# Performance work log

Measured on AMD Instinct MI355X. Metric: run time of the kernel, lower is better.

Reference implementation:

```python
import jax, jax.numpy as jnp
import numpy as np

K, D, H, PD = 512, 512, 512, 128  # nodes, input_dim(=hidden), hidden_dim, pair_dim
P = K * (K - 1)
EPS = 1e-5


def setup_inputs() -> dict:
    key = jax.random.key(0)
    ks = jax.random.split(key, 16)
    s = lambda n: 1.0 / np.sqrt(n)
    return {
        "x": jax.random.normal(ks[0], (K, D), jnp.float32),
        "pair_feats": jax.random.normal(ks[1], (P, PD), jnp.float32),
        "W_att": jax.random.normal(ks[2], (1, 2 * D + PD), jnp.float32) * s(2 * D + PD),
        "b_att": jnp.zeros((1,), jnp.float32),
        "W_obj": jax.random.normal(ks[3], (H, D), jnp.float32) * s(D),
        "b_obj": jnp.zeros((H,), jnp.float32),
        "W_pair": jax.random.normal(ks[4], (H, PD), jnp.float32) * s(PD),
        "b_pair": jnp.zeros((H,), jnp.float32),
        "ln_g": jnp.ones((H,), jnp.float32),
        "ln_b": jnp.zeros((H,), jnp.float32),
        "W1": jax.random.normal(ks[5], (H, H), jnp.float32) * s(H),
        "b1": jnp.zeros((H,), jnp.float32),
        "W2": jax.random.normal(ks[6], (H, H), jnp.float32) * s(H),
        "b2": jnp.zeros((H,), jnp.float32),
    }


def _layernorm(v, g, b):
    mu = jnp.mean(v, axis=-1, keepdims=True)
    var = jnp.mean(jnp.square(v - mu), axis=-1, keepdims=True)
    return g * (v - mu) * jax.lax.rsqrt(var + EPS) + b


def reference(x, pair_feats, W_att, b_att, W_obj, b_obj, W_pair, b_pair,
              ln_g, ln_b, W1, b1, W2, b2):
    k = x.shape[0]
    # j index for each (i, slot t): j = t + (t >= i), i.e. all j != i, ascending
    t = jnp.arange(k - 1)
    j_idx = t[None, :] + (t[None, :] >= jnp.arange(k)[:, None])  # [K, K-1]

    # split the att_mlp weight to avoid materializing cat([x_i, x_j, pair])
    wa, wb, wc = W_att[0, :D], W_att[0, D:2 * D], W_att[0, 2 * D:]
    sa = x @ wa                                           # [K]
    sb = x @ wb                                           # [K]
    pf = pair_feats.reshape(k, k - 1, PD)                 # row-major (i, j!=i)
    sc = jnp.einsum('ktp,p->kt', pf, wc)                  # [K, K-1]
    alpha = jax.nn.sigmoid(sa[:, None] + sb[j_idx] + sc + b_att[0])  # [K, K-1]

    oj = x @ W_obj.T + b_obj                              # [K, H]
    pp = jnp.einsum('ktp,hp->kth', pf, W_pair) + b_pair   # [K, K-1, H]
    messages = jnp.mean(alpha[..., None] * (oj[j_idx] + pp), axis=1)  # [K, H]

    out = _layernorm(x + messages, ln_g, ln_b)
    ffn = jax.nn.relu(out @ W1.T + b1) @ W2.T + b2
    out = _layernorm(out + ffn, ln_g, ln_b)
    return out
```

## Files before the change

### kernel.cpp

```cpp
#include <hip/hip_runtime.h>
#include <math.h>

#define KK 512
#define DD 512
#define HH 512
#define PD 128
#define KM1 511
#define LN_EPS 1e-5f
#define NCHUNK 4
#define CHUNK_T 128

typedef __attribute__((ext_vector_type(8))) short sh8;
typedef __attribute__((ext_vector_type(4))) short sh4;
typedef __attribute__((ext_vector_type(4))) float fx4;

#define MFMA16(a, b, c) __builtin_amdgcn_mfma_f32_16x16x32_bf16(a, b, c, 0, 0, 0)

__device__ __forceinline__ float wave_reduce_sum(float v) {
    #pragma unroll
    for (int off = 32; off > 0; off >>= 1)
        v += __shfl_xor(v, off, 64);
    return v;
}

__device__ __forceinline__ float half_reduce_sum(float v) {
    #pragma unroll
    for (int off = 16; off > 0; off >>= 1)
        v += __shfl_xor(v, off, 64);
    return v;
}

__device__ __forceinline__ short f2bf(float f) {
    unsigned u = __float_as_uint(f);
    u += 0x7fff + ((u >> 16) & 1);
    return (short)(u >> 16);
}

__device__ __forceinline__ sh8 load_cvt8(const float* p) {
    float4 v0 = *(const float4*)p;
    float4 v1 = *(const float4*)(p + 4);
    sh8 r;
    r[0] = f2bf(v0.x); r[1] = f2bf(v0.y); r[2] = f2bf(v0.z); r[3] = f2bf(v0.w);
    r[4] = f2bf(v1.x); r[5] = f2bf(v1.y); r[6] = f2bf(v1.z); r[7] = f2bf(v1.w);
    return r;
}

__global__ __launch_bounds__(256) void prep_sab(
    const float* __restrict__ W_obj, const float* __restrict__ W_pair,
    const float* __restrict__ W1, const float* __restrict__ W2,
    short* __restrict__ W_objb, short* __restrict__ W_pairb,
    short* __restrict__ W1b, short* __restrict__ W2b,
    const float* __restrict__ x, short* __restrict__ xTb,
    const float* __restrict__ W_att, float* __restrict__ sa, float* __restrict__ sb) {
    int bid = blockIdx.x;
    int tid = threadIdx.x;
    if (bid < 832) {
        int i = bid * 256 + tid;
        const float* src; short* dst; int j;
        if (i < 65536)       { src = W_obj;  dst = W_objb;  j = i; }
        else if (i < 81920)  { src = W_pair; dst = W_pairb; j = i - 65536; }
        else if (i < 147456) { src = W1;     dst = W1b;     j = i - 81920; }
        else                 { src = W2;     dst = W2b;     j = i - 147456; }
        float4 v = ((const float4*)src)[j];
        sh4 s;
        s[0] = f2bf(v.x); s[1] = f2bf(v.y); s[2] = f2bf(v.z); s[3] = f2bf(v.w);
        ((sh4*)dst)[j] = s;
    } else if (bid < 1088) {
        int tb = bid - 832;
        int r0 = (tb >> 4) * 32, c0 = (tb & 15) * 32;
        int tx = tid & 31, ty = tid >> 5;
        __shared__ short tileT[32][33];
        #pragma unroll
        for (int i = 0; i < 4; i++) {
            int r = ty + i * 8;
            tileT[tx][r] = f2bf(x[(size_t)(r0 + r) * DD + c0 + tx]);
        }
        __syncthreads();
        #pragma unroll
        for (int i = 0; i < 4; i++) {
            int rr = ty + i * 8;
            xTb[(size_t)(c0 + rr) * KK + r0 + tx] = tileT[rr][tx];
        }
    } else {
        int w = tid >> 6, lane = tid & 63;
        int k = (bid - 1088) * 4 + w;
        const float4* xr = (const float4*)(x + (size_t)k * DD);
        const float4* wa = (const float4*)(W_att);
        const float4* wb = (const float4*)(W_att + DD);
        float pa = 0.f, pb = 0.f;
        #pragma unroll
        for (int i = 0; i < 2; i++) {
            float4 xv = xr[lane + i * 64];
            float4 av = wa[lane + i * 64];
            float4 bv = wb[lane + i * 64];
            pa += xv.x * av.x + xv.y * av.y + xv.z * av.z + xv.w * av.w;
            pb += xv.x * bv.x + xv.y * bv.y + xv.z * bv.z + xv.w * bv.w;
        }
        pa = wave_reduce_sum(pa);
        pb = wave_reduce_sum(pb);
        if (lane == 0) { sa[k] = pa; sb[k] = pb; }
    }
}

__global__ __launch_bounds__(512) void pair_pass_kernel(
    const float* __restrict__ pf, const float* __restrict__ sa,
    const float* __restrict__ sb, const float* __restrict__ W_att,
    const float* __restrict__ b_att, short* __restrict__ Ab,
    float* __restrict__ apf_part, float* __restrict__ asum_part) {
    int k = blockIdx.x;
    int chunk = blockIdx.y;
    int tbase = chunk * CHUNK_T;
    int tid = threadIdx.x;
    int w = tid >> 6, lane = tid & 63;
    int h = lane >> 5, c = lane & 31;
    int g = w * 2 + h;

    float4 wc4 = ((const float4*)(W_att + 2 * DD))[c];
    float sak = sa[k];
    float batt = b_att[0];
    const float4* pfk = (const float4*)(pf + (size_t)k * KM1 * PD);

    float4 v[8];
    int tr[8];
    #pragma unroll
    for (int it = 0; it < 8; it++) {
        int t = tbase + it * 16 + g;
        tr[it] = t;
        int tc = t < KM1 ? t : KM1 - 1;
        v[it] = pfk[(size_t)tc * 32 + c];
    }

    __shared__ float alpha_s[CHUNK_T];
    float a0 = 0.f, a1 = 0.f, a2 = 0.f, a3 = 0.f, asl = 0.f;
    #pragma unroll
    for (int it = 0; it < 8; it++) {
        float part = v[it].x * wc4.x + v[it].y * wc4.y + v[it].z * wc4.z + v[it].w * wc4.w;
        part = half_reduce_sum(part);
        int t = tr[it];
        int j = t + (t >= k);
        int jj = j < KK ? j : KK - 1;
        float z = sak + sb[jj] + part + batt;
        float alpha = (t < KM1) ? 1.f / (1.f + __expf(-z)) : 0.f;
        if (c == 0) alpha_s[it * 16 + g] = alpha;
        a0 += alpha * v[it].x;
        a1 += alpha * v[it].y;
        a2 += alpha * v[it].z;
        a3 += alpha * v[it].w;
        asl += alpha;
    }

    __shared__ float apf_s[16][128];
    __shared__ float asum_s[16];
    apf_s[g][4 * c + 0] = a0;
    apf_s[g][4 * c + 1] = a1;
    apf_s[g][4 * c + 2] = a2;
    apf_s[g][4 * c + 3] = a3;
    if (c == 0) asum_s[g] = asl;
    __syncthreads();
    if (tid < PD) {
        float s = 0.f;
        #pragma unroll
        for (int i = 0; i < 16; i++) s += apf_s[i][tid];
        apf_part[((size_t)chunk * KK + k) * PD + tid] = s;
    }
    if (tid < CHUNK_T) {
        int tt = tbase + tid;
        if (tt < KM1) {
            int j = tt + (tt >= k);
            Ab[(size_t)k * KK + j] = f2bf(alpha_s[tid]);
        }
    }
    if (tid == 0) {
        float s = 0.f;
        #pragma unroll
        for (int i = 0; i < 16; i++) s += asum_s[i];
        asum_part[(size_t)chunk * KK + k] = s;
        if (chunk == 0) Ab[(size_t)k * KK + k] = 0;
    }
}

__global__ __launch_bounds__(128) void k_y(const short* __restrict__ Ab,
                                           const short* __restrict__ xTb,
                                           short* __restrict__ yb) {
    int m0 = blockIdx.y * 32, n0 = blockIdx.x * 32;
    int tid = threadIdx.x;
    int wv = tid >> 6, l = tid & 63;
    int lr = l & 15, lk = (l >> 4) * 8;
    int mw = m0 + wv * 16;
    fx4 acc[2] = {};
    for (int k0 = 0; k0 < KK; k0 += 32) {
        sh8 a  = *(const sh8*)&Ab[(size_t)(mw + lr) * KK + k0 + lk];
        sh8 b0 = *(const sh8*)&xTb[(size_t)(n0 + lr) * KK + k0 + lk];
        sh8 b1 = *(const sh8*)&xTb[(size_t)(n0 + 16 + lr) * KK + k0 + lk];
        acc[0] = MFMA16(a, b0, acc[0]);
        acc[1] = MFMA16(a, b1, acc[1]);
    }
    __shared__ short tile[32][40];
    int lm4 = (l >> 4) * 4;
    #pragma unroll
    for (int cf = 0; cf < 2; cf++)
        #pragma unroll
        for (int r = 0; r < 4; r++)
            tile[wv * 16 + lm4 + r][cf * 16 + lr] = f2bf(acc[cf][r]);
    __syncthreads();
    int row = tid >> 2, co = (tid & 3) * 8;
    *(sh8*)&yb[(size_t)(m0 + row) * KK + n0 + co] = *(sh8*)&tile[row][co];
}

__global__ __launch_bounds__(128) void k_msg(const short* __restrict__ yb,
                                             const short* __restrict__ W_objb,
                                             const float* __restrict__ apf_part,
                                             const short* __restrict__ W_pairb,
                                             float* __restrict__ msg) {
    int m0 = blockIdx.y * 32, n0 = blockIdx.x * 32;
    int tid = threadIdx.x;
    int wv = tid >> 6, l = tid & 63;
    int lr = l & 15, lk = (l >> 4) * 8;
    int mw = m0 + wv * 16;
    fx4 acc[2] = {};
    for (int k0 = 0; k0 < KK; k0 += 32) {
        sh8 a  = *(const sh8*)&yb[(size_t)(mw + lr) * KK + k0 + lk];
        sh8 b0 = *(const sh8*)&W_objb[(size_t)(n0 + lr) * DD + k0 + lk];
        sh8 b1 = *(const sh8*)&W_objb[(size_t)(n0 + 16 + lr) * DD + k0 + lk];
        acc[0] = MFMA16(a, b0, acc[0]);
        acc[1] = MFMA16(a, b1, acc[1]);
    }
    for (int k0 = 0; k0 < PD; k0 += 32) {
        int p = k0 + lk;
        int row = mw + lr;
        float4 u0 = make_float4(0.f, 0.f, 0.f, 0.f);
        float4 u1 = make_float4(0.f, 0.f, 0.f, 0.f);
        #pragma unroll
        for (int cc = 0; cc < NCHUNK; cc++) {
            const float* pp = &apf_part[((size_t)cc * KK + row) * PD + p];
            float4 w0 = *(const float4*)pp;
            float4 w1 = *(const float4*)(pp + 4);
            u0.x += w0.x; u0.y += w0.y; u0.z += w0.z; u0.w += w0.w;
            u1.x += w1.x; u1.y += w1.y; u1.z += w1.z; u1.w += w1.w;
        }
        sh8 a;
        a[0] = f2bf(u0.x); a[1] = f2bf(u0.y); a[2] = f2bf(u0.z); a[3] = f2bf(u0.w);
        a[4] = f2bf(u1.x); a[5] = f2bf(u1.y); a[6] = f2bf(u1.z); a[7] = f2bf(u1.w);
        sh8 b0 = *(const sh8*)&W_pairb[(size_t)(n0 + lr) * PD + p];
        sh8 b1 = *(const sh8*)&W_pairb[(size_t)(n0 + 16 + lr) * PD + p];
        acc[0] = MFMA16(a, b0, acc[0]);
        acc[1] = MFMA16(a, b1, acc[1]);
    }
    __shared__ float tile[32][36];
    int lm4 = (l >> 4) * 4;
    #pragma unroll
    for (int cf = 0; cf < 2; cf++)
        #pragma unroll
        for (int r = 0; r < 4; r++)
            tile[wv * 16 + lm4 + r][cf * 16 + lr] = acc[cf][r];
    __syncthreads();
    for (int q = tid; q < 256; q += 128) {
        int row = q >> 3, c4 = q & 7;
        *(float4*)&msg[(size_t)(m0 + row) * HH + n0 + c4 * 4] = *(float4*)&tile[row][c4 * 4];
    }
}

__global__ __launch_bounds__(128) void ln1_kernel(
    const float* __restrict__ msg, const float* __restrict__ x,
    const float* __restrict__ asum_part, const float* __restrict__ b_pair,
    const float* __restrict__ b_obj, const float* __restrict__ ln_g,
    const float* __restrict__ ln_b, float* __restrict__ out1,
    short* __restrict__ out1b) {
    int k = blockIdx.x;
    int tid = threadIdx.x;
    int wv = tid >> 6, l = tid & 63;
    float as = asum_part[k] + asum_part[KK + k] + asum_part[2 * KK + k] + asum_part[3 * KK + k];
    float4 m  = ((const float4*)(msg + (size_t)k * HH))[tid];
    float4 bp = ((const float4*)b_pair)[tid];
    float4 bo = ((const float4*)b_obj)[tid];
    float4 xr = ((const float4*)(x + (size_t)k * DD))[tid];
    const float inv = 1.0f / (float)KM1;
    float4 v;
    v.x = xr.x + (m.x + as * (bp.x + bo.x)) * inv;
    v.y = xr.y + (m.y + as * (bp.y + bo.y)) * inv;
    v.z = xr.z + (m.z + as * (bp.z + bo.z)) * inv;
    v.w = xr.w + (m.w + as * (bp.w + bo.w)) * inv;
    float s1 = v.x + v.y + v.z + v.w;
    float s2 = v.x * v.x + v.y * v.y + v.z * v.z + v.w * v.w;
    s1 = wave_reduce_sum(s1);
    s2 = wave_reduce_sum(s2);
    __shared__ float r1[2], r2[2];
    if (l == 0) { r1[wv] = s1; r2[wv] = s2; }
    __syncthreads();
    float S1 = r1[0] + r1[1], S2 = r2[0] + r2[1];
    float mu = S1 * (1.0f / HH);
    float var = S2 * (1.0f / HH) - mu * mu;
    float rs = rsqrtf(var + LN_EPS);
    float4 g4 = ((const float4*)ln_g)[tid];
    float4 b4 = ((const float4*)ln_b)[tid];
    float4 o;
    o.x = g4.x * (v.x - mu) * rs + b4.x;
    o.y = g4.y * (v.y - mu) * rs + b4.y;
    o.z = g4.z * (v.z - mu) * rs + b4.z;
    o.w = g4.w * (v.w - mu) * rs + b4.w;
    ((float4*)(out1 + (size_t)k * HH))[tid] = o;
    sh4 s;
    s[0] = f2bf(o.x); s[1] = f2bf(o.y); s[2] = f2bf(o.z); s[3] = f2bf(o.w);
    ((sh4*)(out1b + (size_t)k * HH))[tid] = s;
}

__global__ __launch_bounds__(128) void k_ffn1(const short* __restrict__ out1b,
                                              const short* __restrict__ W1b,
                                              const float* __restrict__ b1,
                                              short* __restrict__ h1b) {
    int m0 = blockIdx.y * 32, n0 = blockIdx.x * 32;
    int tid = threadIdx.x;
    int wv = tid >> 6, l = tid & 63;
    int lr = l & 15, lk = (l >> 4) * 8;
    int mw = m0 + wv * 16;
    fx4 acc[2] = {};
    for (int k0 = 0; k0 < HH; k0 += 32) {
        sh8 a  = *(const sh8*)&out1b[(size_t)(mw + lr) * HH + k0 + lk];
        sh8 b0 = *(const sh8*)&W1b[(size_t)(n0 + lr) * HH + k0 + lk];
        sh8 b1 = *(const sh8*)&W1b[(size_t)(n0 + 16 + lr) * HH + k0 + lk];
        acc[0] = MFMA16(a, b0, acc[0]);
        acc[1] = MFMA16(a, b1, acc[1]);
    }
    __shared__ short tile[32][40];
    int lm4 = (l >> 4) * 4;
    #pragma unroll
    for (int cf = 0; cf < 2; cf++) {
        int col = cf * 16 + lr;
        float bb = b1[n0 + col];
        #pragma unroll
        for (int r = 0; r < 4; r++)
            tile[wv * 16 + lm4 + r][col] = f2bf(fmaxf(acc[cf][r] + bb, 0.f));
    }
    __syncthreads();
    int row = tid >> 2, co = (tid & 3) * 8;
    *(sh8*)&h1b[(size_t)(m0 + row) * HH + n0 + co] = *(sh8*)&tile[row][co];
}

__global__ __launch_bounds__(128) void k_ffn2(const short* __restrict__ h1b,
                                              const short* __restrict__ W2b,
                                              float* __restrict__ ffn) {
    int m0 = blockIdx.y * 32, n0 = blockIdx.x * 32;
    int tid = threadIdx.x;
    int wv = tid >> 6, l = tid & 63;
    int lr = l & 15, lk = (l >> 4) * 8;
    int mw = m0 + wv * 16;
    fx4 acc[2] = {};
    for (int k0 = 0; k0 < HH; k0 += 32) {
        sh8 a  = *(const sh8*)&h1b[(size_t)(mw + lr) * HH + k0 + lk];
        sh8 b0 = *(const sh8*)&W2b[(size_t)(n0 + lr) * HH + k0 + lk];
        sh8 b1 = *(const sh8*)&W2b[(size_t)(n0 + 16 + lr) * HH + k0 + lk];
        acc[0] = MFMA16(a, b0, acc[0]);
        acc[1] = MFMA16(a, b1, acc[1]);
    }
    __shared__ float tile[32][36];
    int lm4 = (l >> 4) * 4;
    #pragma unroll
    for (int cf = 0; cf < 2; cf++)
        #pragma unroll
        for (int r = 0; r < 4; r++)
            tile[wv * 16 + lm4 + r][cf * 16 + lr] = acc[cf][r];
    __syncthreads();
    for (int q = tid; q < 256; q += 128) {
        int row = q >> 3, c4 = q & 7;
        *(float4*)&ffn[(size_t)(m0 + row) * HH + n0 + c4 * 4] = *(float4*)&tile[row][c4 * 4];
    }
}

__global__ __launch_bounds__(128) void ln2_kernel(
    const float* __restrict__ ffn, const float* __restrict__ out1,
    const float* __restrict__ b2, const float* __restrict__ ln_g,
    const float* __restrict__ ln_b, float* __restrict__ out) {
    int k = blockIdx.x;
    int tid = threadIdx.x;
    int wv = tid >> 6, l = tid & 63;
    float4 f  = ((const float4*)(ffn + (size_t)k * HH))[tid];
    float4 xr = ((const float4*)(out1 + (size_t)k * HH))[tid];
    float4 bb = ((const float4*)b2)[tid];
    float4 v;
    v.x = xr.x + f.x + bb.x;
    v.y = xr.y + f.y + bb.y;
    v.z = xr.z + f.z + bb.z;
    v.w = xr.w + f.w + bb.w;
    float s1 = v.x + v.y + v.z + v.w;
    float s2 = v.x * v.x + v.y * v.y + v.z * v.z + v.w * v.w;
    s1 = wave_reduce_sum(s1);
    s2 = wave_reduce_sum(s2);
    __shared__ float r1[2], r2[2];
    if (l == 0) { r1[wv] = s1; r2[wv] = s2; }
    __syncthreads();
    float S1 = r1[0] + r1[1], S2 = r2[0] + r2[1];
    float mu = S1 * (1.0f / HH);
    float var = S2 * (1.0f / HH) - mu * mu;
    float rs = rsqrtf(var + LN_EPS);
    float4 g4 = ((const float4*)ln_g)[tid];
    float4 b4 = ((const float4*)ln_b)[tid];
    float4 o;
    o.x = g4.x * (v.x - mu) * rs + b4.x;
    o.y = g4.y * (v.y - mu) * rs + b4.y;
    o.z = g4.z * (v.z - mu) * rs + b4.z;
    o.w = g4.w * (v.w - mu) * rs + b4.w;
    ((float4*)(out + (size_t)k * HH))[tid] = o;
}

extern "C" void kernel_launch(void* const* d_in, const int* in_sizes, int n_in,
                              void* d_out, int out_size, void* d_ws, size_t ws_size,
                              hipStream_t stream) {
    const float* x          = (const float*)d_in[0];
    const float* pair_feats = (const float*)d_in[1];
    const float* W_att      = (const float*)d_in[2];
    const float* b_att      = (const float*)d_in[3];
    const float* W_obj      = (const float*)d_in[4];
    const float* b_obj      = (const float*)d_in[5];
    const float* W_pair     = (const float*)d_in[6];
    const float* b_pair     = (const float*)d_in[7];
    const float* ln_g       = (const float*)d_in[8];
    const float* ln_b       = (const float*)d_in[9];
    const float* W1         = (const float*)d_in[10];
    const float* b1         = (const float*)d_in[11];
    const float* W2         = (const float*)d_in[12];
    const float* b2         = (const float*)d_in[13];
    float* out = (float*)d_out;

    const size_t MAT = (size_t)KK * HH;
    float* ws        = (float*)d_ws;
    float* sa        = ws;
    float* sb        = sa + KK;
    float* asum_part = sb + KK;
    float* apf_part  = asum_part + NCHUNK * KK;
    float* msg       = apf_part + (size_t)NCHUNK * KK * PD;
    float* out1      = msg + MAT;
    float* ffn       = out1 + MAT;
    float* psink     = ffn + MAT;
    short* Ab        = (short*)(psink + NCHUNK * KK);
    short* xTb       = Ab + MAT;
    short* W_objb    = xTb + MAT;
    short* W_pairb   = W_objb + MAT;
    short* W1b       = W_pairb + (size_t)HH * PD;
    short* W2b       = W1b + MAT;
    short* yb        = W2b + MAT;
    short* out1b     = yb + MAT;
    short* h1b       = out1b + MAT;

    prep_sab<<<1216, 256, 0, stream>>>(W_obj, W_pair, W1, W2, W_objb, W_pairb, W1b, W2b,
                                       x, xTb, W_att, sa, sb);
    pair_pass_kernel<<<dim3(512, NCHUNK), 512, 0, stream>>>(pair_feats, sa, sb, W_att, b_att,
                                                            Ab, apf_part, asum_part);
    k_y<<<dim3(16, 16), 128, 0, stream>>>(Ab, xTb, yb);
    k_msg<<<dim3(16, 16), 128, 0, stream>>>(yb, W_objb, apf_part, W_pairb, msg);
    ln1_kernel<<<512, 128, 0, stream>>>(msg, x, asum_part, b_pair, b_obj, ln_g, ln_b, out1, out1b);
    k_ffn1<<<dim3(16, 16), 128, 0, stream>>>(out1b, W1b, b1, h1b);
    k_ffn2<<<dim3(16, 16), 128, 0, stream>>>(h1b, W2b, ffn);
    ln2_kernel<<<512, 128, 0, stream>>>(ffn, out1, b2, ln_g, ln_b, out);
}
```

Measured before the change: 63.00 us.

## Fuse LayerNorm1 into FFN1 and convert weights to bf16 inside GEMMs

Drops the separate weight-to-bf16 conversion pass; the GEMM kernels now load fp32 weights and convert them in registers. LayerNorm1 is folded into the FFN1 prologue: each block recomputes the normalized rows into shared memory. The final kernel recomputes LN1 from msg so it can apply the residual and LN2 without storing out1. This removes two launches and several intermediate buffers, at the cost of redundant LN1 work across the 16 column blocks and doubled fp32 weight traffic per GEMM tile.

Result: slower. 87.99 us (+39.7%).

```diff
diff --git a/kernel.cpp b/kernel.cpp
--- a/kernel.cpp
+++ b/kernel.cpp
@@ -46,28 +46,12 @@
 }
 
 __global__ __launch_bounds__(256) void prep_sab(
-    const float* __restrict__ W_obj, const float* __restrict__ W_pair,
-    const float* __restrict__ W1, const float* __restrict__ W2,
-    short* __restrict__ W_objb, short* __restrict__ W_pairb,
-    short* __restrict__ W1b, short* __restrict__ W2b,
     const float* __restrict__ x, short* __restrict__ xTb,
     const float* __restrict__ W_att, float* __restrict__ sa, float* __restrict__ sb) {
     int bid = blockIdx.x;
     int tid = threadIdx.x;
-    if (bid < 832) {
-        int i = bid * 256 + tid;
-        const float* src; short* dst; int j;
-        if (i < 65536)       { src = W_obj;  dst = W_objb;  j = i; }
-        else if (i < 81920)  { src = W_pair; dst = W_pairb; j = i - 65536; }
-        else if (i < 147456) { src = W1;     dst = W1b;     j = i - 81920; }
-        else                 { src = W2;     dst = W2b;     j = i - 147456; }
-        float4 v = ((const float4*)src)[j];
-        sh4 s;
-        s[0] = f2bf(v.x); s[1] = f2bf(v.y); s[2] = f2bf(v.z); s[3] = f2bf(v.w);
-        ((sh4*)dst)[j] = s;
-    } else if (bid < 1088) {
-        int tb = bid - 832;
-        int r0 = (tb >> 4) * 32, c0 = (tb & 15) * 32;
+    if (bid < 256) {
+        int r0 = (bid >> 4) * 32, c0 = (bid & 15) * 32;
         int tx = tid & 31, ty = tid >> 5;
         __shared__ short tileT[32][33];
         #pragma unroll
@@ -83,7 +67,7 @@
         }
     } else {
         int w = tid >> 6, lane = tid & 63;
-        int k = (bid - 1088) * 4 + w;
+        int k = (bid - 256) * 4 + w;
         const float4* xr = (const float4*)(x + (size_t)k * DD);
         const float4* wa = (const float4*)(W_att);
         const float4* wb = (const float4*)(W_att + DD);
@@ -208,9 +192,9 @@
 }
 
 __global__ __launch_bounds__(128) void k_msg(const short* __restrict__ yb,
-                                             const short* __restrict__ W_objb,
+                                             const float* __restrict__ W_obj,
                                              const float* __restrict__ apf_part,
-                                             const short* __restrict__ W_pairb,
+                                             const float* __restrict__ W_pair,
                                              float* __restrict__ msg) {
     int m0 = blockIdx.y * 32, n0 = blockIdx.x * 32;
     int tid = threadIdx.x;
@@ -220,8 +204,8 @@
     fx4 acc[2] = {};
     for (int k0 = 0; k0 < KK; k0 += 32) {
         sh8 a  = *(const sh8*)&yb[(size_t)(mw + lr) * KK + k0 + lk];
-        sh8 b0 = *(const sh8*)&W_objb[(size_t)(n0 + lr) * DD + k0 + lk];
-        sh8 b1 = *(const sh8*)&W_objb[(size_t)(n0 + 16 + lr) * DD + k0 + lk];
+        sh8 b0 = load_cvt8(&W_obj[(size_t)(n0 + lr) * DD + k0 + lk]);
+        sh8 b1 = load_cvt8(&W_obj[(size_t)(n0 + 16 + lr) * DD + k0 + lk]);
         acc[0] = MFMA16(a, b0, acc[0]);
         acc[1] = MFMA16(a, b1, acc[1]);
     }
@@ -241,8 +225,8 @@
         sh8 a;
         a[0] = f2bf(u0.x); a[1] = f2bf(u0.y); a[2] = f2bf(u0.z); a[3] = f2bf(u0.w);
         a[4] = f2bf(u1.x); a[5] = f2bf(u1.y); a[6] = f2bf(u1.z); a[7] = f2bf(u1.w);
-        sh8 b0 = *(const sh8*)&W_pairb[(size_t)(n0 + lr) * PD + p];
-        sh8 b1 = *(const sh8*)&W_pairb[(size_t)(n0 + 16 + lr) * PD + p];
+        sh8 b0 = load_cvt8(&W_pair[(size_t)(n0 + lr) * PD + p]);
+        sh8 b1 = load_cvt8(&W_pair[(size_t)(n0 + 16 + lr) * PD + p]);
         acc[0] = MFMA16(a, b0, acc[0]);
         acc[1] = MFMA16(a, b1, acc[1]);
     }
@@ -260,12 +244,126 @@
     }
 }
 
-__global__ __launch_bounds__(128) void ln1_kernel(
+__global__ __launch_bounds__(128) void k_ffn1(
     const float* __restrict__ msg, const float* __restrict__ x,
     const float* __restrict__ asum_part, const float* __restrict__ b_pair,
     const float* __restrict__ b_obj, const float* __restrict__ ln_g,
-    const float* __restrict__ ln_b, float* __restrict__ out1,
-    short* __restrict__ out1b) {
+    const float* __restrict__ ln_b, const float* __restrict__ W1,
+    const float* __restrict__ b1, short* __restrict__ h1b) {
+    int m0 = blockIdx.y * 32, n0 = blockIdx.x * 32;
+    int tid = threadIdx.x;
+    __shared__ short a_tile[32][514];
+
+    {
+        int r = tid >> 2, q = tid & 3;
+        int grow = m0 + r;
+        float as = asum_part[grow] + asum_part[KK + grow] +
+                   asum_part[2 * KK + grow] + asum_part[3 * KK + grow];
+        const float4* m4  = (const float4*)(msg + (size_t)grow * HH);
+        const float4* x4  = (const float4*)(x + (size_t)grow * DD);
+        const float4* bp4 = (const float4*)b_pair;
+        const float4* bo4 = (const float4*)b_obj;
+        const float inv = 1.0f / (float)KM1;
+        float s1 = 0.f, s2 = 0.f;
+        #pragma unroll 8
+        for (int i = 0; i < 32; i++) {
+            int idx = q + i * 4;
+            float4 m = m4[idx], xr = x4[idx], bp = bp4[idx], bo = bo4[idx];
+            float vx = xr.x + (m.x + as * (bp.x + bo.x)) * inv;
+            float vy = xr.y + (m.y + as * (bp.y + bo.y)) * inv;
+            float vz = xr.z + (m.z + as * (bp.z + bo.z)) * inv;
+            float vw = xr.w + (m.w + as * (bp.w + bo.w)) * inv;
+            s1 += vx + vy + vz + vw;
+            s2 += vx * vx + vy * vy + vz * vz + vw * vw;
+        }
+        s1 += __shfl_xor(s1, 1, 64); s1 += __shfl_xor(s1, 2, 64);
+        s2 += __shfl_xor(s2, 1, 64); s2 += __shfl_xor(s2, 2, 64);
+        float mu = s1 * (1.0f / HH);
+        float var = s2 * (1.0f / HH) - mu * mu;
+        float rs = rsqrtf(var + LN_EPS);
+        const float4* g4p = (const float4*)ln_g;
+        const float4* b4p = (const float4*)ln_b;
+        #pragma unroll 8
+        for (int i = 0; i < 32; i++) {
+            int idx = q + i * 4;
+            float4 m = m4[idx], xr = x4[idx], bp = bp4[idx], bo = bo4[idx];
+            float4 g = g4p[idx], bl = b4p[idx];
+            float vx = xr.x + (m.x + as * (bp.x + bo.x)) * inv;
+            float vy = xr.y + (m.y + as * (bp.y + bo.y)) * inv;
+            float vz = xr.z + (m.z + as * (bp.z + bo.z)) * inv;
+            float vw = xr.w + (m.w + as * (bp.w + bo.w)) * inv;
+            sh4 o;
+            o[0] = f2bf(g.x * (vx - mu) * rs + bl.x);
+            o[1] = f2bf(g.y * (vy - mu) * rs + bl.y);
+            o[2] = f2bf(g.z * (vz - mu) * rs + bl.z);
+            o[3] = f2bf(g.w * (vw - mu) * rs + bl.w);
+            *(sh4*)&a_tile[r][idx * 4] = o;
+        }
+    }
+    __syncthreads();
+
+    int wv = tid >> 6, l = tid & 63;
+    int lr = l & 15, lk = (l >> 4) * 8;
+    fx4 acc[2] = {};
+    for (int k0 = 0; k0 < HH; k0 += 32) {
+        sh8 a  = *(const sh8*)&a_tile[wv * 16 + lr][k0 + lk];
+        sh8 b0 = load_cvt8(&W1[(size_t)(n0 + lr) * HH + k0 + lk]);
+        sh8 b1v = load_cvt8(&W1[(size_t)(n0 + 16 + lr) * HH + k0 + lk]);
+        acc[0] = MFMA16(a, b0, acc[0]);
+        acc[1] = MFMA16(a, b1v, acc[1]);
+    }
+    __syncthreads();
+    __shared__ short tile[32][40];
+    int lm4 = (l >> 4) * 4;
+    #pragma unroll
+    for (int cf = 0; cf < 2; cf++) {
+        int col = cf * 16 + lr;
+        float bb = b1[n0 + col];
+        #pragma unroll
+        for (int r = 0; r < 4; r++)
+            tile[wv * 16 + lm4 + r][col] = f2bf(fmaxf(acc[cf][r] + bb, 0.f));
+    }
+    __syncthreads();
+    int row = tid >> 2, co = (tid & 3) * 8;
+    *(sh8*)&h1b[(size_t)(m0 + row) * HH + n0 + co] = *(sh8*)&tile[row][co];
+}
+
+__global__ __launch_bounds__(128) void k_ffn2(const short* __restrict__ h1b,
+                                              const float* __restrict__ W2,
+                                              float* __restrict__ ffn) {
+    int m0 = blockIdx.y * 32, n0 = blockIdx.x * 32;
+    int tid = threadIdx.x;
+    int wv = tid >> 6, l = tid & 63;
+    int lr = l & 15, lk = (l >> 4) * 8;
+    int mw = m0 + wv * 16;
+    fx4 acc[2] = {};
+    for (int k0 = 0; k0 < HH; k0 += 32) {
+        sh8 a  = *(const sh8*)&h1b[(size_t)(mw + lr) * HH + k0 + lk];
+        sh8 b0 = load_cvt8(&W2[(size_t)(n0 + lr) * HH + k0 + lk]);
+        sh8 b1 = load_cvt8(&W2[(size_t)(n0 + 16 + lr) * HH + k0 + lk]);
+        acc[0] = MFMA16(a, b0, acc[0]);
+        acc[1] = MFMA16(a, b1, acc[1]);
+    }
+    __shared__ float tile[32][36];
+    int lm4 = (l >> 4) * 4;
+    #pragma unroll
+    for (int cf = 0; cf < 2; cf++)
+        #pragma unroll
+        for (int r = 0; r < 4; r++)
+            tile[wv * 16 + lm4 + r][cf * 16 + lr] = acc[cf][r];
+    __syncthreads();
+    for (int q = tid; q < 256; q += 128) {
+        int row = q >> 3, c4 = q & 7;
+        *(float4*)&ffn[(size_t)(m0 + row) * HH + n0 + c4 * 4] = *(float4*)&tile[row][c4 * 4];
+    }
+}
+
+__global__ __launch_bounds__(128) void ln2_rec(
+    const float* __restrict__ msg, const float* __restrict__ x,
+    const float* __restrict__ asum_part, const float* __restrict__ b_pair,
+    const float* __restrict__ b_obj, const float* __restrict__ ffn,
+    const float* __restrict__ b2, const float* __restrict__ ln_g,
+    const float* __restrict__ ln_b, float* __restrict__ out) {
     int k = blockIdx.x;
     int tid = threadIdx.x;
     int wv = tid >> 6, l = tid & 63;
@@ -275,13 +373,13 @@
     float4 bo = ((const float4*)b_obj)[tid];
     float4 xr = ((const float4*)(x + (size_t)k * DD))[tid];
     const float inv = 1.0f / (float)KM1;
-    float4 v;
-    v.x = xr.x + (m.x + as * (bp.x + bo.x)) * inv;
-    v.y = xr.y + (m.y + as * (bp.y + bo.y)) * inv;
-    v.z = xr.z + (m.z + as * (bp.z + bo.z)) * inv;
-    v.w = xr.w + (m.w + as * (bp.w + bo.w)) * inv;
-    float s1 = v.x + v.y + v.z + v.w;
-    float s2 = v.x * v.x + v.y * v.y + v.z * v.z + v.w * v.w;
+    float4 v1;
+    v1.x = xr.x + (m.x + as * (bp.x + bo.x)) * inv;
+    v1.y = xr.y + (m.y + as * (bp.y + bo.y)) * inv;
+    v1.z = xr.z + (m.z + as * (bp.z + bo.z)) * inv;
+    v1.w = xr.w + (m.w + as * (bp.w + bo.w)) * inv;
+    float s1 = v1.x + v1.y + v1.z + v1.w;
+    float s2 = v1.x * v1.x + v1.y * v1.y + v1.z * v1.z + v1.w * v1.w;
     s1 = wave_reduce_sum(s1);
     s2 = wave_reduce_sum(s2);
     __shared__ float r1[2], r2[2];
@@ -293,112 +391,35 @@
     float rs = rsqrtf(var + LN_EPS);
     float4 g4 = ((const float4*)ln_g)[tid];
     float4 b4 = ((const float4*)ln_b)[tid];
+    float4 o1;
+    o1.x = g4.x * (v1.x - mu) * rs + b4.x;
+    o1.y = g4.y * (v1.y - mu) * rs + b4.y;
+    o1.z = g4.z * (v1.z - mu) * rs + b4.z;
+    o1.w = g4.w * (v1.w - mu) * rs + b4.w;
+
+    float4 f  = ((const float4*)(ffn + (size_t)k * HH))[tid];
+    float4 bb = ((const float4*)b2)[tid];
+    float4 v2;
+    v2.x = o1.x + f.x + bb.x;
+    v2.y = o1.y + f.y + bb.y;
+    v2.z = o1.z + f.z + bb.z;
+    v2.w = o1.w + f.w + bb.w;
+    float t1 = v2.x + v2.y + v2.z + v2.w;
+    float t2 = v2.x * v2.x + v2.y * v2.y + v2.z * v2.z + v2.w * v2.w;
+    t1 = wave_reduce_sum(t1);
+    t2 = wave_reduce_sum(t2);
+    __syncthreads();
+    if (l == 0) { r1[wv] = t1; r2[wv] = t2; }
+    __syncthreads();
+    float T1 = r1[0] + r1[1], T2 = r2[0] + r2[1];
+    float mu2 = T1 * (1.0f / HH);
+    float var2 = T2 * (1.0f / HH) - mu2 * mu2;
+    float rs2 = rsqrtf(var2 + LN_EPS);
     float4 o;
-    o.x = g4.x * (v.x - mu) * rs + b4.x;
-    o.y = g4.y * (v.y - mu) * rs + b4.y;
-    o.z = g4.z * (v.z - mu) * rs + b4.z;
-    o.w = g4.w * (v.w - mu) * rs + b4.w;
-    ((float4*)(out1 + (size_t)k * HH))[tid] = o;
-    sh4 s;
-    s[0] = f2bf(o.x); s[1] = f2bf(o.y); s[2] = f2bf(o.z); s[3] = f2bf(o.w);
-    ((sh4*)(out1b + (size_t)k * HH))[tid] = s;
-}
-
-__global__ __launch_bounds__(128) void k_ffn1(const short* __restrict__ out1b,
-                                              const short* __restrict__ W1b,
-                                              const float* __restrict__ b1,
-                                              short* __restrict__ h1b) {
-    int m0 = blockIdx.y * 32, n0 = blockIdx.x * 32;
-    int tid = threadIdx.x;
-    int wv = tid >> 6, l = tid & 63;
-    int lr = l & 15, lk = (l >> 4) * 8;
-    int mw = m0 + wv * 16;
-    fx4 acc[2] = {};
-    for (int k0 = 0; k0 < HH; k0 += 32) {
-        sh8 a  = *(const sh8*)&out1b[(size_t)(mw + lr) * HH + k0 + lk];
-        sh8 b0 = *(const sh8*)&W1b[(size_t)(n0 + lr) * HH + k0 + lk];
-        sh8 b1 = *(const sh8*)&W1b[(size_t)(n0 + 16 + lr) * HH + k0 + lk];
-        acc[0] = MFMA16(a, b0, acc[0]);
-        acc[1] = MFMA16(a, b1, acc[1]);
-    }
-    __shared__ short tile[32][40];
-    int lm4 = (l >> 4) * 4;
-    #pragma unroll
-    for (int cf = 0; cf < 2; cf++) {
-        int col = cf * 16 + lr;
-        float bb = b1[n0 + col];
-        #pragma unroll
-        for (int r = 0; r < 4; r++)
-            tile[wv * 16 + lm4 + r][col] = f2bf(fmaxf(acc[cf][r] + bb, 0.f));
-    }
-    __syncthreads();
-    int row = tid >> 2, co = (tid & 3) * 8;
-    *(sh8*)&h1b[(size_t)(m0 + row) * HH + n0 + co] = *(sh8*)&tile[row][co];
-}
-
-__global__ __launch_bounds__(128) void k_ffn2(const short* __restrict__ h1b,
-                                              const short* __restrict__ W2b,
-                                              float* __restrict__ ffn) {
-    int m0 = blockIdx.y * 32, n0 = blockIdx.x * 32;
-    int tid = threadIdx.x;
-    int wv = tid >> 6, l = tid & 63;
-    int lr = l & 15, lk = (l >> 4) * 8;
-    int mw = m0 + wv * 16;
-    fx4 acc[2] = {};
-    for (int k0 = 0; k0 < HH; k0 += 32) {
-        sh8 a  = *(const sh8*)&h1b[(size_t)(mw + lr) * HH + k0 + lk];
-        sh8 b0 = *(const sh8*)&W2b[(size_t)(n0 + lr) * HH + k0 + lk];
-        sh8 b1 = *(const sh8*)&W2b[(size_t)(n0 + 16 + lr) * HH + k0 + lk];
-        acc[0] = MFMA16(a, b0, acc[0]);
-        acc[1] = MFMA16(a, b1, acc[1]);
-    }
-    __shared__ float tile[32][36];
-    int lm4 = (l >> 4) * 4;
-    #pragma unroll
-    for (int cf = 0; cf < 2; cf++)
-        #pragma unroll
-        for (int r = 0; r < 4; r++)
-            tile[wv * 16 + lm4 + r][cf * 16 + lr] = acc[cf][r];
-    __syncthreads();
-    for (int q = tid; q < 256; q += 128) {
-        int row = q >> 3, c4 = q & 7;
-        *(float4*)&ffn[(size_t)(m0 + row) * HH + n0 + c4 * 4] = *(float4*)&tile[row][c4 * 4];
-    }
-}
-
-__global__ __launch_bounds__(128) void ln2_kernel(
-    const float* __restrict__ ffn, const float* __restrict__ out1,
-    const float* __restrict__ b2, const float* __restrict__ ln_g,
-    const float* __restrict__ ln_b, float* __restrict__ out) {
-    int k = blockIdx.x;
-    int tid = threadIdx.x;
-    int wv = tid >> 6, l = tid & 63;
-    float4 f  = ((const float4*)(ffn + (size_t)k * HH))[tid];
-    float4 xr = ((const float4*)(out1 + (size_t)k * HH))[tid];
-    float4 bb = ((const float4*)b2)[tid];
-    float4 v;
-    v.x = xr.x + f.x + bb.x;
-    v.y = xr.y + f.y + bb.y;
-    v.z = xr.z + f.z + bb.z;
-    v.w = xr.w + f.w + bb.w;
-    float s1 = v.x + v.y + v.z + v.w;
-    float s2 = v.x * v.x + v.y * v.y + v.z * v.z + v.w * v.w;
-    s1 = wave_reduce_sum(s1);
-    s2 = wave_reduce_sum(s2);
-    __shared__ float r1[2], r2[2];
-    if (l == 0) { r1[wv] = s1; r2[wv] = s2; }
-    __syncthreads();
-    float S1 = r1[0] + r1[1], S2 = r2[0] + r2[1];
-    float mu = S1 * (1.0f / HH);
-    float var = S2 * (1.0f / HH) - mu * mu;
-    float rs = rsqrtf(var + LN_EPS);
-    float4 g4 = ((const float4*)ln_g)[tid];
-    float4 b4 = ((const float4*)ln_b)[tid];
-    float4 o;
-    o.x = g4.x * (v.x - mu) * rs + b4.x;
-    o.y = g4.y * (v.y - mu) * rs + b4.y;
-    o.z = g4.z * (v.z - mu) * rs + b4.z;
-    o.w = g4.w * (v.w - mu) * rs + b4.w;
+    o.x = g4.x * (v2.x - mu2) * rs2 + b4.x;
+    o.y = g4.y * (v2.y - mu2) * rs2 + b4.y;
+    o.z = g4.z * (v2.z - mu2) * rs2 + b4.z;
+    o.w = g4.w * (v2.w - mu2) * rs2 + b4.w;
     ((float4*)(out + (size_t)k * HH))[tid] = o;
 }
 
@@ -428,27 +449,20 @@
     float* asum_part = sb + KK;
     float* apf_part  = asum_part + NCHUNK * KK;
     float* msg       = apf_part + (size_t)NCHUNK * KK * PD;
-    float* out1      = msg + MAT;
-    float* ffn       = out1 + MAT;
-    float* psink     = ffn + MAT;
-    short* Ab        = (short*)(psink + NCHUNK * KK);
+    float* ffn       = msg + MAT;
+    short* Ab        = (short*)(ffn + MAT);
     short* xTb       = Ab + MAT;
-    short* W_objb    = xTb + MAT;
-    short* W_pairb   = W_objb + MAT;
-    short* W1b       = W_pairb + (size_t)HH * PD;
-    short* W2b       = W1b + MAT;
-    short* yb        = W2b + MAT;
-    short* out1b     = yb + MAT;
-    short* h1b       = out1b + MAT;
-
-    prep_sab<<<1216, 256, 0, stream>>>(W_obj, W_pair, W1, W2, W_objb, W_pairb, W1b, W2b,
-                                       x, xTb, W_att, sa, sb);
+    short* yb        = xTb + MAT;
+    short* h1b       = yb + MAT;
+
+    prep_sab<<<384, 256, 0, stream>>>(x, xTb, W_att, sa, sb);
     pair_pass_kernel<<<dim3(512, NCHUNK), 512, 0, stream>>>(pair_feats, sa, sb, W_att, b_att,
                                                             Ab, apf_part, asum_part);
     k_y<<<dim3(16, 16), 128, 0, stream>>>(Ab, xTb, yb);
-    k_msg<<<dim3(16, 16), 128, 0, stream>>>(yb, W_objb, apf_part, W_pairb, msg);
-    ln1_kernel<<<512, 128, 0, stream>>>(msg, x, asum_part, b_pair, b_obj, ln_g, ln_b, out1, out1b);
-    k_ffn1<<<dim3(16, 16), 128, 0, stream>>>(out1b, W1b, b1, h1b);
-    k_ffn2<<<dim3(16, 16), 128, 0, stream>>>(h1b, W2b, ffn);
-    ln2_kernel<<<512, 128, 0, stream>>>(ffn, out1, b2, ln_g, ln_b, out);
-}
+    k_msg<<<dim3(16, 16), 128, 0, stream>>>(yb, W_obj, apf_part, W_pair, msg);
+    k_ffn1<<<dim3(16, 16), 128, 0, stream>>>(msg, x, asum_part, b_pair, b_obj,
+                                             ln_g, ln_b, W1, b1, h1b);
+    k_ffn2<<<dim3(16, 16), 128, 0, stream>>>(h1b, W2, ffn);
+    ln2_rec<<<512, 128, 0, stream>>>(msg, x, asum_part, b_pair, b_obj, ffn, b2,
+                                     ln_g, ln_b, out);
+}
```
